# Kernel tuning notes

Measured on AMD Instinct MI355X. Metric: run time of the kernel, lower is better.

The kernel has to match this reference:

```python
import jax, jax.numpy as jnp
from jax import lax
import numpy as np

HEAD_SIZE = 64
D_MIX = 32
D_DECAY = 64
D_GATE = 64


def setup_inputs() -> dict:
    key = jax.random.key(0)
    B, T, C = 4, 2048, 1024
    H = C // HEAD_SIZE
    ks = jax.random.split(key, 24)
    n = lambda i, shape, s=1.0: (jax.random.normal(ks[i], shape, dtype=jnp.float32) * s)
    return {
        "x": n(0, (B, T, C)),
        "maa_x": n(1, (C,), 0.1), "maa_w": n(2, (C,), 0.1), "maa_k": n(3, (C,), 0.1),
        "maa_v": n(4, (C,), 0.1), "maa_r": n(5, (C,), 0.1), "maa_g": n(6, (C,), 0.1),
        "maa_w1": n(7, (C, 5 * D_MIX), 0.01), "maa_w2": n(8, (5, D_MIX, C), 0.01),
        "Wr": n(9, (C, C), C ** -0.5), "Wk": n(10, (C, C), C ** -0.5),
        "Wv": n(11, (C, C), C ** -0.5), "Wo": n(12, (C, C), C ** -0.5),
        "gate_w1": n(13, (C, D_GATE), 0.01), "gate_w2": n(14, (D_GATE, C), 0.01),
        "time_decay": n(15, (C,), 1.0) - 4.0,
        "decay_w1": n(16, (C, D_DECAY), 0.01), "decay_w2": n(17, (D_DECAY, C), 0.01),
        "u": n(18, (H, HEAD_SIZE), 0.1),
        "ln_g": jnp.ones((C,), jnp.float32), "ln_b": jnp.zeros((C,), jnp.float32),
    }


def _wkv6(r, k, v, w, u):
    # r,k,v: [B,T,C]; w: decay (already exp(-exp(.))) [B,T,C]; u: [H,N]
    B, T, C = r.shape
    N = HEAD_SIZE
    H = C // N
    to_h = lambda a: a.reshape(B, T, H, N).transpose(1, 0, 2, 3)  # [T,B,H,N]
    rT, kT, vT, wT = map(to_h, (r, k, v, w))

    def step(S, inp):  # S: [B,H,N,N] (key_dim i x value_dim j)
        rt, kt, vt, wt = inp
        kv = kt[..., :, None] * vt[..., None, :]            # [B,H,N,N]
        y = jnp.einsum('bhi,bhij->bhj', rt, S + u[None, :, :, None] * kv)
        S = wt[..., None] * S + kv
        return S, y

    S0 = jnp.zeros((B, H, N, N), r.dtype)
    _, y = lax.scan(step, S0, (rT, kT, vT, wT))
    return y.transpose(1, 0, 2, 3).reshape(B, T, C)


def reference(x, maa_x, maa_w, maa_k, maa_v, maa_r, maa_g, maa_w1, maa_w2,
              Wr, Wk, Wv, Wo, gate_w1, gate_w2, time_decay, decay_w1, decay_w2,
              u, ln_g, ln_b):
    B, T, C = x.shape
    H, N = C // HEAD_SIZE, HEAD_SIZE
    # time shift: prepend zero row, drop last (ZeroPad2d((0,0,1,-1)))
    xx = jnp.concatenate([jnp.zeros_like(x[:, :1]), x[:, :-1]], axis=1) - x
    xxx = x + xx * maa_x
    lora = jnp.tanh(xxx @ maa_w1).reshape(B, T, 5, D_MIX)
    m = jnp.einsum('btfd,fdc->fbtc', lora, maa_w2)  # [5,B,T,C]
    mw, mk, mv, mr, mg = m[0], m[1], m[2], m[3], m[4]
    xw = x + xx * (maa_w + mw)
    xk = x + xx * (maa_k + mk)
    xv = x + xx * (maa_v + mv)
    xr = x + xx * (maa_r + mr)
    xg = x + xx * (maa_g + mg)
    r = xr @ Wr
    k = xk @ Wk
    v = xv @ Wv
    g = jnp.tanh(xg @ gate_w1) @ gate_w2
    w = time_decay + jnp.tanh(xw @ decay_w1) @ decay_w2
    wdec = jnp.exp(-jnp.exp(w))  # decay applied inside the CUDA kernel
    y = _wkv6(r, k, v, wdec, u)
    # GroupNorm over heads, eps = 1e-5 * HEAD_SIZE_DIVISOR**2 = 6.4e-4
    yh = y.reshape(B, T, H, N)
    mu = yh.mean(-1, keepdims=True)
    var = yh.var(-1, keepdims=True)
    yn = ((yh - mu) / jnp.sqrt(var + 6.4e-4)).reshape(B, T, C) * ln_g + ln_b
    return (yn * g) @ Wo
```

## Files before the change

### kernel.cpp

```cpp
#include <hip/hip_runtime.h>
#include <hip/hip_bf16.h>
#include <stdint.h>

typedef __hip_bfloat16 bf16;
typedef __attribute__((ext_vector_type(8))) short bf16x8;
typedef __attribute__((ext_vector_type(4))) float f32x4;

#define CC 1024
#define TT 2048
#define BB 4
#define BT 8192
#define HH 16
#define NN 64

#define MFMA(a, b, c) __builtin_amdgcn_mfma_f32_16x16x32_bf16(a, b, c, 0, 0, 0)

#define GLD(g, l) __builtin_amdgcn_global_load_lds( \
    (const __attribute__((address_space(1))) void*)(g), \
    (__attribute__((address_space(3))) void*)(l), 16, 0, 0)

__device__ __forceinline__ short f2bs(float f) {
    bf16 h = __float2bfloat16(f);
    return *reinterpret_cast<short*>(&h);
}
__device__ __forceinline__ float bs2f(short s) {
    bf16 h = *reinterpret_cast<bf16*>(&s);
    return __bfloat162float(h);
}

__device__ __forceinline__ size_t blk_idx(int m, int k, int ktiles) {
    return ((size_t)(m >> 8) * ktiles + (k >> 6)) * 16384
         + ((k >> 3) & 7) * 2048 + (m & 255) * 8 + (k & 7);
}

__device__ __forceinline__ size_t blk128_idx(int m, int k, int ktiles) {
    return ((size_t)(m >> 7) * ktiles + (k >> 6)) * 8192
         + ((k >> 3) & 7) * 1024 + (m & 127) * 8 + (k & 7);
}

__device__ __forceinline__ size_t hb_idx(int m, int n) {
    return ((((size_t)(m >> 11) << 4) + (n >> 6)) * 2048 + (m & 2047)) * 64
         + (n & 63);
}

template <typename EPI>
__device__ __forceinline__ void gemm128(short* As, short* Bs,
                                        const bf16* __restrict__ A, int lda,
                                        const bf16* __restrict__ Bt, int ldb,
                                        int kiters, int m0, int n0, EPI epi)
{
    const int tid = threadIdx.x;
    const int l   = tid & 63, wv = tid >> 6;
    const int wm  = wv >> 1, wn = wv & 1;
    const int q   = l >> 4, lr = l & 15;
    const int row = tid & 127, kg1 = tid >> 7;

    f32x4 acc[4][4] = {};

    const bf16* ga = A  + (size_t)(m0 + row) * lda + kg1 * 8;
    const bf16* gb = Bt + (size_t)(n0 + row) * ldb + kg1 * 8;
    short* la1 = As + tid * 8;
    short* la2 = As + (tid + 256) * 8;
    short* lb1 = Bs + tid * 8;
    short* lb2 = Bs + (tid + 256) * 8;

    for (int kb = 0; kb < kiters; ++kb) {
        __syncthreads();
        const bf16* gak = ga + kb * 32;
        const bf16* gbk = gb + kb * 32;
        GLD(gak,      la1);
        GLD(gak + 16, la2);
        GLD(gbk,      lb1);
        GLD(gbk + 16, lb2);
        __syncthreads();
        bf16x8 af[4], bfb[4];
#pragma unroll
        for (int mt = 0; mt < 4; ++mt)
            af[mt] = *(const bf16x8*)(As + (q * 128 + wm * 64 + mt * 16 + lr) * 8);
#pragma unroll
        for (int nt = 0; nt < 4; ++nt)
            bfb[nt] = *(const bf16x8*)(Bs + (q * 128 + wn * 64 + nt * 16 + lr) * 8);
#pragma unroll
        for (int mt = 0; mt < 4; ++mt)
#pragma unroll
            for (int nt = 0; nt < 4; ++nt)
                acc[mt][nt] = MFMA(af[mt], bfb[nt], acc[mt][nt]);
    }
#pragma unroll
    for (int mt = 0; mt < 4; ++mt)
#pragma unroll
        for (int nt = 0; nt < 4; ++nt)
#pragma unroll
            for (int rr = 0; rr < 4; ++rr)
                epi(m0 + wm * 64 + mt * 16 + q * 4 + rr,
                    n0 + wn * 64 + nt * 16 + lr, acc[mt][nt][rr]);
}

template <typename EPI>
__device__ __forceinline__ void gemm128b(short* As, short* Bs,
                                         const bf16* __restrict__ A,
                                         const bf16* __restrict__ Bt,
                                         int kiters, int m0, int n0, EPI epi)
{
    const int tid = threadIdx.x;
    const int l   = tid & 63, wv = tid >> 6;
    const int wm  = wv >> 1, wn = wv & 1;
    const int q   = l >> 4, lr = l & 15;

    f32x4 acc[4][4] = {};

    const bf16* ga = A  + (size_t)(m0 >> 7) * 16 * 8192 + tid * 8;
    const bf16* gb = Bt + (size_t)(n0 >> 7) * 16 * 8192 + tid * 8;

    auto stage = [&](int kb, int u) {
        const bf16* gak = ga + (size_t)kb * 8192;
        const bf16* gbk = gb + (size_t)kb * 8192;
        short* la = As + u * 8192 + tid * 8;
        short* lb = Bs + u * 8192 + tid * 8;
        GLD(gak,        la);
        GLD(gak + 2048, la + 2048);
        GLD(gak + 4096, la + 4096);
        GLD(gak + 6144, la + 6144);
        GLD(gbk,        lb);
        GLD(gbk + 2048, lb + 2048);
        GLD(gbk + 4096, lb + 4096);
        GLD(gbk + 6144, lb + 6144);
    };

    __syncthreads();
    stage(0, 0);
    __syncthreads();
    for (int kb = 0; kb < kiters; ++kb) {
        const int cur = kb & 1;
        if (kb + 1 < kiters) stage(kb + 1, cur ^ 1);
        const short* Ac = As + cur * 8192;
        const short* Bc = Bs + cur * 8192;
        bf16x8 af[2][4], bfb[2][4];
#pragma unroll
        for (int hh = 0; hh < 2; ++hh) {
#pragma unroll
            for (int mt = 0; mt < 4; ++mt)
                af[hh][mt] = *(const bf16x8*)(Ac +
                    ((q + hh * 4) * 128 + wm * 64 + mt * 16 + lr) * 8);
#pragma unroll
            for (int nt = 0; nt < 4; ++nt)
                bfb[hh][nt] = *(const bf16x8*)(Bc +
                    ((q + hh * 4) * 128 + wn * 64 + nt * 16 + lr) * 8);
        }
        __builtin_amdgcn_s_setprio(1);
#pragma unroll
        for (int mt = 0; mt < 4; ++mt)
#pragma unroll
            for (int nt = 0; nt < 4; ++nt) {
                acc[mt][nt] = MFMA(af[0][mt], bfb[0][nt], acc[mt][nt]);
                acc[mt][nt] = MFMA(af[1][mt], bfb[1][nt], acc[mt][nt]);
            }
        __builtin_amdgcn_s_setprio(0);
        __syncthreads();
    }
#pragma unroll
    for (int mt = 0; mt < 4; ++mt)
#pragma unroll
        for (int nt = 0; nt < 4; ++nt)
#pragma unroll
            for (int rr = 0; rr < 4; ++rr)
                epi(m0 + wm * 64 + mt * 16 + q * 4 + rr,
                    n0 + wn * 64 + nt * 16 + lr, acc[mt][nt][rr]);
}

template <typename EPI>
__device__ __forceinline__ void gemm256(short* As, short* Bs,
                                        const bf16* __restrict__ A,
                                        const bf16* __restrict__ Bt,
                                        int kiters, int m0, int n0, EPI epi)
{
    const int tid = threadIdx.x;
    const int l   = tid & 63, wv = tid >> 6;
    const int wm  = wv >> 2, wn = wv & 3;
    const int q   = l >> 4, lr = l & 15;

    f32x4 acc[8][4] = {};

    const bf16* ga = A  + (size_t)(m0 >> 8) * 16 * 16384 + tid * 8;
    const bf16* gb = Bt + (size_t)(n0 >> 8) * 16 * 16384 + tid * 8;

    auto stage = [&](int kb, int u) {
        const bf16* gak = ga + (size_t)kb * 16384;
        const bf16* gbk = gb + (size_t)kb * 16384;
        short* la = As + u * 16384 + tid * 8;
        short* lb = Bs + u * 16384 + tid * 8;
        GLD(gak,         la);
        GLD(gak + 4096,  la + 4096);
        GLD(gak + 8192,  la + 8192);
        GLD(gak + 12288, la + 12288);
        GLD(gbk,         lb);
        GLD(gbk + 4096,  lb + 4096);
        GLD(gbk + 8192,  lb + 8192);
        GLD(gbk + 12288, lb + 12288);
    };

    __syncthreads();
    stage(0, 0);
    __syncthreads();
    for (int kb = 0; kb < kiters; ++kb) {
        const int cur = kb & 1;
        if (kb + 1 < kiters) stage(kb + 1, cur ^ 1);
        const short* Ac = As + cur * 16384;
        const short* Bc = Bs + cur * 16384;
#pragma unroll
        for (int hh = 0; hh < 2; ++hh) {
            bf16x8 af[8], bfb[4];
#pragma unroll
            for (int mt = 0; mt < 8; ++mt)
                af[mt] = *(const bf16x8*)(Ac +
                    ((q + hh * 4) * 256 + wm * 128 + mt * 16 + lr) * 8);
#pragma unroll
            for (int nt = 0; nt < 4; ++nt)
                bfb[nt] = *(const bf16x8*)(Bc +
                    ((q + hh * 4) * 256 + wn * 64 + nt * 16 + lr) * 8);
            __builtin_amdgcn_s_setprio(1);
#pragma unroll
            for (int mt = 0; mt < 8; ++mt)
#pragma unroll
                for (int nt = 0; nt < 4; ++nt)
                    acc[mt][nt] = MFMA(af[mt], bfb[nt], acc[mt][nt]);
            __builtin_amdgcn_s_setprio(0);
        }
        __syncthreads();
    }
#pragma unroll
    for (int mt = 0; mt < 8; ++mt)
#pragma unroll
        for (int nt = 0; nt < 4; ++nt)
#pragma unroll
            for (int rr = 0; rr < 4; ++rr)
                epi(m0 + wm * 128 + mt * 16 + q * 4 + rr,
                    n0 + wn * 64 + nt * 16 + lr, acc[mt][nt][rr]);
}

template <typename EPI>
__device__ __forceinline__ void gemmHid(short* As, short* Bs,
                                        const bf16* __restrict__ A,
                                        const bf16* __restrict__ Bt, int ldb,
                                        int kiters, int m0, EPI epi)
{
    const int tid = threadIdx.x;
    const int l   = tid & 63, wv = tid >> 6;
    const int q   = l >> 4, lr = l & 15;
    const int row64 = tid & 63, kg8 = tid >> 6;

    f32x4 acc[2][4] = {};

    const bf16* ga = A + (size_t)(m0 >> 8) * 16 * 16384 + tid * 8;
    const bf16* gb = Bt + (size_t)row64 * ldb + kg8 * 8;

    auto stage = [&](int kb, int u) {
        const bf16* gak = ga + (size_t)kb * 16384;
        short* la = As + u * 16384 + tid * 8;
        GLD(gak,         la);
        GLD(gak + 4096,  la + 4096);
        GLD(gak + 8192,  la + 8192);
        GLD(gak + 12288, la + 12288);
        GLD(gb + kb * 64, Bs + u * 4096 + tid * 8);
    };

    __syncthreads();
    stage(0, 0);
    __syncthreads();
    for (int kb = 0; kb < kiters; ++kb) {
        const int cur = kb & 1;
        if (kb + 1 < kiters) stage(kb + 1, cur ^ 1);
        const short* Ac = As + cur * 16384;
        const short* Bc = Bs + cur * 4096;
        bf16x8 af[2][2], bfb[2][4];
#pragma unroll
        for (int hh = 0; hh < 2; ++hh) {
#pragma unroll
            for (int mt = 0; mt < 2; ++mt)
                af[hh][mt] = *(const bf16x8*)(Ac +
                    ((q + hh * 4) * 256 + wv * 32 + mt * 16 + lr) * 8);
#pragma unroll
            for (int nt = 0; nt < 4; ++nt)
                bfb[hh][nt] = *(const bf16x8*)(Bc +
                    ((q + hh * 4) * 64 + nt * 16 + lr) * 8);
        }
#pragma unroll
        for (int mt = 0; mt < 2; ++mt)
#pragma unroll
            for (int nt = 0; nt < 4; ++nt) {
                acc[mt][nt] = MFMA(af[0][mt], bfb[0][nt], acc[mt][nt]);
                acc[mt][nt] = MFMA(af[1][mt], bfb[1][nt], acc[mt][nt]);
            }
        __syncthreads();
    }
#pragma unroll
    for (int mt = 0; mt < 2; ++mt)
#pragma unroll
        for (int nt = 0; nt < 4; ++nt)
#pragma unroll
            for (int rr = 0; rr < 4; ++rr)
                epi(m0 + wv * 32 + mt * 16 + q * 4 + rr,
                    nt * 16 + lr, acc[mt][nt][rr]);
}

__global__ __launch_bounds__(256) void k_prep_all(
    const float* __restrict__ Wr, const float* __restrict__ Wk,
    const float* __restrict__ Wv, const float* __restrict__ Wo,
    const float* __restrict__ maa_w1, const float* __restrict__ gate_w1,
    const float* __restrict__ decay_w1, const float* __restrict__ gate_w2,
    const float* __restrict__ decay_w2, const float* __restrict__ maa_w2,
    const float* __restrict__ mw, const float* __restrict__ mk,
    const float* __restrict__ mv, const float* __restrict__ mr,
    const float* __restrict__ mg, const float* __restrict__ x,
    const float* __restrict__ maa_x,
    bf16* __restrict__ WT3, bf16* __restrict__ WoT, bf16* __restrict__ w1T,
    bf16* __restrict__ w1T2, bf16* __restrict__ w2T2, bf16* __restrict__ w2T5,
    float* __restrict__ maas, bf16* __restrict__ xxx,
    bf16* __restrict__ xb, bf16* __restrict__ xxb)
{
    __shared__ float tile[32][33];
    int idx = blockIdx.x;
    if (idx >= 4900) {
        size_t i = ((size_t)(idx - 4900) * 256 + threadIdx.x) * 4;
        int cc = i & (CC - 1);
        int t  = (i >> 10) & (TT - 1);
        float4 xm = *(const float4*)(x + i);
        float4 xp = t ? *(const float4*)(x + i - CC)
                      : make_float4(0.f, 0.f, 0.f, 0.f);
        float4 ax = *(const float4*)(maa_x + cc);
        float xxv[4] = {xp.x - xm.x, xp.y - xm.y, xp.z - xm.z, xp.w - xm.w};
        float xmv[4] = {xm.x, xm.y, xm.z, xm.w};
        float axv[4] = {ax.x, ax.y, ax.z, ax.w};
#pragma unroll
        for (int e = 0; e < 4; ++e) {
            xb[i + e]  = __float2bfloat16(xmv[e]);
            xxb[i + e] = __float2bfloat16(xxv[e]);
            xxx[i + e] = __float2bfloat16(xmv[e] + xxv[e] * axv[e]);
        }
        return;
    }
    const float* src; bf16* dst; int rows, cols_in, tx_;
    int blkmode = 0;
    if (idx < 4096) {
        int s = idx >> 10; idx &= 1023;
        src = (s == 0) ? Wr : (s == 1) ? Wk : (s == 2) ? Wv : Wo;
        dst = (s == 3) ? WoT : WT3 + (size_t)s * CC * CC;
        blkmode = (s == 3) ? 2 : 1;
        rows = CC; cols_in = CC; tx_ = 32;
    } else if (idx < 4352) { idx -= 4096; src = maa_w1;  dst = w1T;  rows = CC; cols_in = 160; tx_ = 8; }
    else if (idx < 4480)   { idx -= 4352; src = gate_w1; dst = w1T2; rows = CC; cols_in = 64;  tx_ = 4; }
    else if (idx < 4608)   { idx -= 4480; src = decay_w1; dst = w1T2 + 128 * CC; rows = CC; cols_in = 64; tx_ = 4; }
    else if (idx < 4672)   { idx -= 4608; src = gate_w2;  dst = w2T2;           rows = 64; cols_in = CC; tx_ = 32; }
    else if (idx < 4736)   { idx -= 4672; src = decay_w2; dst = w2T2 + CC * 64; rows = 64; cols_in = CC; tx_ = 32; }
    else if (idx < 4896)   { idx -= 4736; int f = idx >> 5; idx &= 31;
                             src = maa_w2 + (size_t)f * 32 * CC;
                             dst = w2T5 + (size_t)f * CC * 32; rows = 32; cols_in = CC; tx_ = 32; }
    else {
        int i = (idx - 4896) * 256 + threadIdx.x;
        if (i < CC) {
            maas[i]          = mw[i];
            maas[CC + i]     = mk[i];
            maas[2 * CC + i] = mv[i];
            maas[3 * CC + i] = mr[i];
            maas[4 * CC + i] = mg[i];
        }
        return;
    }
    int bx = idx % tx_, by = idx / tx_;
    int c0 = bx * 32, r0 = by * 32;
    int tx = threadIdx.x & 31, ty = threadIdx.x >> 5;
    for (int i = ty; i < 32; i += 8) {
        int cc2 = c0 + tx;
        tile[i][tx] = (cc2 < cols_in) ? src[(size_t)(r0 + i) * cols_in + cc2] : 0.f;
    }
    __syncthreads();
    if (blkmode == 1) {
        for (int i = ty; i < 32; i += 8) {
            int R = c0 + i, C = r0 + tx;
            dst[blk_idx(R, C, 16)] = __float2bfloat16(tile[tx][i]);
        }
    } else if (blkmode == 2) {
        for (int i = ty; i < 32; i += 8) {
            int R = c0 + i, C = r0 + tx;
            dst[blk128_idx(R, C, 16)] = __float2bfloat16(tile[tx][i]);
        }
    } else {
        for (int i = ty; i < 32; i += 8)
            dst[(size_t)(c0 + i) * rows + r0 + tx] = __float2bfloat16(tile[tx][i]);
    }
}

__global__ __launch_bounds__(256) void g_lora(const bf16* __restrict__ xxx,
                                              const bf16* __restrict__ w1T,
                                              bf16* __restrict__ L)
{
    __shared__ __align__(16) short lds[8192];
    int m0 = blockIdx.x * 128, n0 = blockIdx.y * 128;
    gemm128(lds, lds + 4096, xxx, CC, w1T, CC, CC / 32, m0, n0,
            [&](int m, int n, float v) {
                if (n < 160) L[(size_t)m * 160 + n] = __float2bfloat16(tanhf(v));
            });
}

__global__ __launch_bounds__(256) void g_xvar(const bf16* __restrict__ L,
                                              const bf16* __restrict__ w2T,
                                              const float* __restrict__ maas,
                                              const bf16* __restrict__ xb,
                                              const bf16* __restrict__ xxb,
                                              bf16* __restrict__ xvars)
{
    __shared__ __align__(16) short lds[8192];
    int m0 = blockIdx.x * 128, n0 = blockIdx.y * 128;
    for (int f = 0; f < 5; ++f) {
        const bf16* A  = L + f * 32;
        const bf16* Bt = w2T + (size_t)f * CC * 32;
        const float* maa = maas + f * CC;
        bf16* out = xvars + (size_t)f * BT * CC;
        gemm128(lds, lds + 4096, A, 160, Bt, 32, 1, m0, n0,
                [&](int m, int n, float v) {
                    float xm = __bfloat162float(xb[(size_t)m * CC + n]);
                    float xx = __bfloat162float(xxb[(size_t)m * CC + n]);
                    out[blk_idx(m, n, 16)] =
                        __float2bfloat16(xm + xx * (maa[n] + v));
                });
    }
}

__global__ __launch_bounds__(512) void g_rkv5(const bf16* __restrict__ xvars,
                                              const bf16* __restrict__ WT,
                                              const bf16* __restrict__ w1T2,
                                              bf16* __restrict__ rkv,
                                              bf16* __restrict__ hid)
{
    __shared__ __align__(16) short lds[65536];
    int bid = blockIdx.x;
    if (bid < 384) {
        int swz = (bid & 7) * 48 + (bid >> 3);
        int z  = swz >> 7;
        int r2 = swz & 127;
        int n0 = (r2 >> 5) * 256;
        int m0 = (r2 & 31) * 256;
        int f = (z == 0) ? 3 : z;
        const bf16* A  = xvars + (size_t)f * BT * CC;
        const bf16* Bt = WT + (size_t)z * CC * CC;
        bf16* out = rkv + (size_t)z * BT * CC;
        gemm256(lds, lds + 32768, A, Bt, CC / 64, m0, n0,
                [&](int m, int n, float v) {
                    out[hb_idx(m, n)] = __float2bfloat16(v);
                });
    } else {
        int hb = bid - 384;
        int zz = hb >> 5, mi = hb & 31;
        const bf16* A  = xvars + (size_t)(zz == 0 ? 4 : 0) * BT * CC;
        const bf16* Bt = w1T2 + (size_t)zz * 128 * CC;
        bf16* out = hid + (size_t)zz * BT * 64;
        gemmHid(lds, lds + 32768, A, Bt, CC, CC / 64, mi * 256,
                [&](int m, int n, float v) {
                    out[(size_t)m * 64 + n] = __float2bfloat16(tanhf(v));
                });
    }
}

__global__ __launch_bounds__(256) void k_wkv_p1(const bf16* __restrict__ r,
                                                const bf16* __restrict__ kk,
                                                const bf16* __restrict__ vv,
                                                const bf16* __restrict__ hidW,
                                                const bf16* __restrict__ w2d,
                                                const float* __restrict__ td,
                                                const float* __restrict__ u,
                                                bf16* __restrict__ y,
                                                bf16* __restrict__ RTg,
                                                short* __restrict__ Mg,
                                                float* __restrict__ plg)
{
    constexpr int PW = 65, PB = 72;
    __shared__ __align__(16) char smem[16640 + 3 * 9216 + 768];
    float* LW = (float*)smem;
    short* VT = (short*)smem;
    short* RT = (short*)(smem + 16640);
    short* KT = (short*)(smem + 16640 + 9216);
    short* AT = KT;
    short* KH = (short*)(smem + 16640 + 2 * 9216);
    short* HT = KT;
    short* WD = KH;
    float* SU = (float*)(smem + 16640 + 3 * 9216);
    float* SD = SU + 64;

    const int tid = threadIdx.x;
    const int lane = tid & 63, wq = tid >> 6;
    const int row = tid >> 2, g = tid & 3, j0 = g * 16;
    const int l15 = lane & 15, q = lane >> 4;
    const int bh = blockIdx.x >> 5, c = blockIdx.x & 31;
    const int b = bh >> 4, h = bh & 15;
    const int t0 = c * 64;
    const int bt0 = b * TT + t0;
    const size_t hbb = (size_t)bh * TT * NN;
    const size_t cb = (size_t)blockIdx.x * 4096;

    if (tid < 64) SU[tid] = u[h * NN + tid];

#pragma unroll
    for (int rnd = 0; rnd < 2; ++rnd) {
        int ee = rnd * 256 + tid;
        int rw = ee >> 3, c8 = (ee & 7) * 8;
        *(bf16x8*)(HT + rw * PB + c8) =
            *(const bf16x8*)(hidW + (size_t)(bt0 + rw) * 64 + c8);
        *(bf16x8*)(WD + rw * PB + c8) =
            *(const bf16x8*)(w2d + (size_t)(h * 64 + rw) * 64 + c8);
    }
    const size_t gb = hbb + (size_t)(t0 + row) * 64 + j0;
    bf16x8 r0 = *(const bf16x8*)(r + gb),  r1 = *(const bf16x8*)(r + gb + 8);
    bf16x8 k0 = *(const bf16x8*)(kk + gb), k1 = *(const bf16x8*)(kk + gb + 8);
    bf16x8 v0 = *(const bf16x8*)(vv + gb), v1 = *(const bf16x8*)(vv + gb + 8);
    float tdv[4];
#pragma unroll
    for (int ct = 0; ct < 4; ++ct) tdv[ct] = td[h * 64 + ct * 16 + l15];
    __syncthreads();
    {
        bf16x8 aH0 = *(const bf16x8*)(HT + (wq * 16 + l15) * PB + q * 8);
        bf16x8 aH1 = *(const bf16x8*)(HT + (wq * 16 + l15) * PB + q * 8 + 32);
        f32x4 lwa[4] = {};
#pragma unroll
        for (int ct = 0; ct < 4; ++ct) {
            bf16x8 bW0 = *(const bf16x8*)(WD + (ct * 16 + l15) * PB + q * 8);
            bf16x8 bW1 = *(const bf16x8*)(WD + (ct * 16 + l15) * PB + q * 8 + 32);
            lwa[ct] = MFMA(aH0, bW0, lwa[ct]);
            lwa[ct] = MFMA(aH1, bW1, lwa[ct]);
        }
#pragma unroll
        for (int ct = 0; ct < 4; ++ct)
#pragma unroll
            for (int rr = 0; rr < 4; ++rr) {
                int t = wq * 16 + q * 4 + rr, j = ct * 16 + l15;
                LW[t * PW + j] = -expf(tdv[ct] + lwa[ct][rr]);
            }
    }
    __syncthreads();
    for (int jj = 0; jj < 16; ++jj) {
        int j = wq * 16 + jj;
        float xv = LW[lane * PW + j];
#pragma unroll
        for (int d = 1; d < 64; d <<= 1) {
            float t2 = __shfl_up(xv, d);
            if (lane >= d) xv += t2;
        }
        LW[lane * PW + j] = xv;
    }
    __syncthreads();
    float rF[16], kF[16];
#pragma unroll
    for (int c2 = 0; c2 < 8; ++c2) {
        rF[c2] = bs2f(r0[c2]); rF[8 + c2] = bs2f(r1[c2]);
        kF[c2] = bs2f(k0[c2]); kF[8 + c2] = bs2f(k1[c2]);
    }
    float cwp[16], cwm[16], cwL[16];
#pragma unroll
    for (int c2 = 0; c2 < 16; ++c2) {
        cwp[c2] = LW[row * PW + j0 + c2];
        cwm[c2] = row ? LW[(row - 1) * PW + j0 + c2] : 0.f;
        cwL[c2] = LW[63 * PW + j0 + c2];
    }
    bf16x8 w0, w1;
#pragma unroll
    for (int c2 = 0; c2 < 8; ++c2) {
        w0[c2] = f2bs(rF[c2] * expf(cwm[c2]));
        w1[c2] = f2bs(rF[8 + c2] * expf(cwm[8 + c2]));
    }
    *(bf16x8*)(RT + row * PB + j0)     = w0;
    *(bf16x8*)(RT + row * PB + j0 + 8) = w1;
    *(bf16x8*)((short*)RTg + cb + row * 64 + j0)     = w0;
    *(bf16x8*)((short*)RTg + cb + row * 64 + j0 + 8) = w1;
#pragma unroll
    for (int c2 = 0; c2 < 8; ++c2) {
        w0[c2] = f2bs(kF[c2] * expf(-cwp[c2]));
        w1[c2] = f2bs(kF[8 + c2] * expf(-cwp[8 + c2]));
    }
    *(bf16x8*)(KT + row * PB + j0)     = w0;
    *(bf16x8*)(KT + row * PB + j0 + 8) = w1;
#pragma unroll
    for (int c2 = 0; c2 < 16; ++c2)
        KH[(j0 + c2) * PB + row] = f2bs(kF[c2] * expf(cwL[c2] - cwp[c2]));
    if (tid < 64) plg[(size_t)blockIdx.x * 64 + tid] = expf(LW[63 * PW + tid]);
    float dpart = 0.f;
#pragma unroll
    for (int c2 = 0; c2 < 16; ++c2)
        dpart = fmaf(rF[c2] * kF[c2], SU[j0 + c2], dpart);
    dpart += __shfl_xor(dpart, 1);
    dpart += __shfl_xor(dpart, 2);
    if (g == 0) SD[row] = dpart;
    __syncthreads();
#pragma unroll
    for (int c2 = 0; c2 < 8; ++c2) {
        VT[(j0 + c2) * PB + row]     = v0[c2];
        VT[(j0 + 8 + c2) * PB + row] = v1[c2];
    }
    bf16x8 aF0 = *(const bf16x8*)(RT + (wq * 16 + l15) * PB + q * 8);
    bf16x8 aF1 = *(const bf16x8*)(RT + (wq * 16 + l15) * PB + q * 8 + 32);
    f32x4 Am[4] = {};
#pragma unroll
    for (int ct = 0; ct < 4; ++ct) {
        bf16x8 bF0 = *(const bf16x8*)(KT + (ct * 16 + l15) * PB + q * 8);
        bf16x8 bF1 = *(const bf16x8*)(KT + (ct * 16 + l15) * PB + q * 8 + 32);
        Am[ct] = MFMA(aF0, bF0, Am[ct]);
        Am[ct] = MFMA(aF1, bF1, Am[ct]);
    }
    __syncthreads();
#pragma unroll
    for (int ct = 0; ct < 4; ++ct)
#pragma unroll
        for (int rr = 0; rr < 4; ++rr) {
            int s = wq * 16 + q * 4 + rr, p = ct * 16 + l15;
            float vA = Am[ct][rr];
            vA = (p > s) ? 0.f : (p == s ? SD[s] : vA);
            AT[s * PB + p] = f2bs(vA);
        }
    __syncthreads();
    f32x4 Y[4] = {}, M[4] = {};
    bf16x8 aA0 = *(const bf16x8*)(AT + (wq * 16 + l15) * PB + q * 8);
    bf16x8 aA1 = *(const bf16x8*)(AT + (wq * 16 + l15) * PB + q * 8 + 32);
    bf16x8 aV0 = *(const bf16x8*)(VT + (wq * 16 + l15) * PB + q * 8);
    bf16x8 aV1 = *(const bf16x8*)(VT + (wq * 16 + l15) * PB + q * 8 + 32);
#pragma unroll
    for (int ct = 0; ct < 4; ++ct) {
        bf16x8 bV0 = *(const bf16x8*)(VT + (ct * 16 + l15) * PB + q * 8);
        bf16x8 bV1 = *(const bf16x8*)(VT + (ct * 16 + l15) * PB + q * 8 + 32);
        Y[ct] = MFMA(aA0, bV0, Y[ct]);
        Y[ct] = MFMA(aA1, bV1, Y[ct]);
        bf16x8 bK0 = *(const bf16x8*)(KH + (ct * 16 + l15) * PB + q * 8);
        bf16x8 bK1 = *(const bf16x8*)(KH + (ct * 16 + l15) * PB + q * 8 + 32);
        M[ct] = MFMA(aV0, bK0, M[ct]);
        M[ct] = MFMA(aV1, bK1, M[ct]);
    }
#pragma unroll
    for (int ct = 0; ct < 4; ++ct)
#pragma unroll
        for (int rr = 0; rr < 4; ++rr) {
            int s = wq * 16 + q * 4 + rr;
            y[hbb + (size_t)(t0 + s) * 64 + ct * 16 + l15] =
                __float2bfloat16(Y[ct][rr]);
            Mg[cb + (size_t)s * 64 + ct * 16 + l15] = f2bs(M[ct][rr]);
        }
}

__global__ __launch_bounds__(256) void k_wkv_p2(const short* __restrict__ Mg,
                                                const float* __restrict__ plg,
                                                bf16* __restrict__ Sg)
{
    int bh = blockIdx.x >> 4, part = blockIdx.x & 15;
    int i = part * 4 + (threadIdx.x >> 6), j = threadIdx.x & 63;
    float S = 0.f;
    size_t eb = (size_t)bh * 32 * 4096 + (size_t)i * 64 + j;
    size_t pb = (size_t)bh * 32 * 64 + j;
    for (int c = 0; c < 32; ++c) {
        Sg[eb + (size_t)c * 4096] = __float2bfloat16(S);
        S = plg[pb + (size_t)c * 64] * S + bs2f(Mg[eb + (size_t)c * 4096]);
    }
}

__global__ __launch_bounds__(256) void k_wkv_p3(const bf16* __restrict__ RTg,
                                                const bf16* __restrict__ Sg,
                                                const bf16* __restrict__ y,
                                                const bf16* __restrict__ hidG,
                                                const bf16* __restrict__ w2g,
                                                const float* __restrict__ ln_g,
                                                const float* __restrict__ ln_b,
                                                bf16* __restrict__ A2)
{
    constexpr int PB = 72;
    __shared__ __align__(16) short BufA[64 * PB], BufB[64 * PB];
    const int tid = threadIdx.x;
    const int lane = tid & 63, wq = tid >> 6;
    const int l15 = lane & 15, q = lane >> 4;
    const int bh = blockIdx.x >> 5, c = blockIdx.x & 31;
    const int b = bh >> 4, h = bh & 15;
    const int t0 = c * 64;
    const int bt0 = b * TT + t0;
    const size_t hbb = (size_t)bh * TT * NN;
    const size_t cb = (size_t)blockIdx.x * 4096;

#pragma unroll
    for (int rnd = 0; rnd < 2; ++rnd) {
        int ee = rnd * 256 + tid;
        int rw = ee >> 3, c8 = (ee & 7) * 8;
        *(bf16x8*)(BufA + rw * PB + c8) =
            *(const bf16x8*)(hidG + (size_t)(bt0 + rw) * 64 + c8);
        *(bf16x8*)(BufB + rw * PB + c8) =
            *(const bf16x8*)(w2g + (size_t)(h * 64 + rw) * 64 + c8);
    }
    __syncthreads();
    f32x4 G[4] = {};
    {
        bf16x8 aH0 = *(const bf16x8*)(BufA + (wq * 16 + l15) * PB + q * 8);
        bf16x8 aH1 = *(const bf16x8*)(BufA + (wq * 16 + l15) * PB + q * 8 + 32);
#pragma unroll
        for (int ct = 0; ct < 4; ++ct) {
            bf16x8 bW0 = *(const bf16x8*)(BufB + (ct * 16 + l15) * PB + q * 8);
            bf16x8 bW1 = *(const bf16x8*)(BufB + (ct * 16 + l15) * PB + q * 8 + 32);
            G[ct] = MFMA(aH0, bW0, G[ct]);
            G[ct] = MFMA(aH1, bW1, G[ct]);
        }
    }
    __syncthreads();
#pragma unroll
    for (int rnd = 0; rnd < 2; ++rnd) {
        int ee = rnd * 256 + tid;
        int rw = ee >> 3, c8 = (ee & 7) * 8;
        *(bf16x8*)(BufA + rw * PB + c8) =
            *(const bf16x8*)((const short*)RTg + cb + rw * 64 + c8);
        *(bf16x8*)(BufB + rw * PB + c8) =
            *(const bf16x8*)((const short*)Sg + cb + rw * 64 + c8);
    }
    __syncthreads();

    f32x4 Yc[4];
#pragma unroll
    for (int ct = 0; ct < 4; ++ct)
#pragma unroll
        for (int rr = 0; rr < 4; ++rr) {
            int s = wq * 16 + q * 4 + rr;
            Yc[ct][rr] = __bfloat162float(
                y[hbb + (size_t)(t0 + s) * 64 + ct * 16 + l15]);
        }
    bf16x8 aF0 = *(const bf16x8*)(BufA + (wq * 16 + l15) * PB + q * 8);
    bf16x8 aF1 = *(const bf16x8*)(BufA + (wq * 16 + l15) * PB + q * 8 + 32);
#pragma unroll
    for (int ct = 0; ct < 4; ++ct) {
        bf16x8 bS0 = *(const bf16x8*)(BufB + (ct * 16 + l15) * PB + q * 8);
        bf16x8 bS1 = *(const bf16x8*)(BufB + (ct * 16 + l15) * PB + q * 8 + 32);
        Yc[ct] = MFMA(aF0, bS0, Yc[ct]);
        Yc[ct] = MFMA(aF1, bS1, Yc[ct]);
    }
#pragma unroll
    for (int rr = 0; rr < 4; ++rr) {
        float s1 = 0.f, s2 = 0.f;
#pragma unroll
        for (int ct = 0; ct < 4; ++ct) {
            float vA = Yc[ct][rr];
            s1 += vA; s2 += vA * vA;
        }
#pragma unroll
        for (int o = 1; o < 16; o <<= 1) {
            s1 += __shfl_xor(s1, o);
            s2 += __shfl_xor(s2, o);
        }
        float mu  = s1 * (1.f / 64.f);
        float var = s2 * (1.f / 64.f) - mu * mu;
        float rstd = rsqrtf(var + 6.4e-4f);
        int s = wq * 16 + q * 4 + rr;
#pragma unroll
        for (int ct = 0; ct < 4; ++ct) {
            int ch = h * NN + ct * 16 + l15;
            float yn = (Yc[ct][rr] - mu) * rstd;
            float out = (yn * ln_g[ch] + ln_b[ch]) * G[ct][rr];
            A2[blk128_idx(bt0 + s, ch, 16)] = __float2bfloat16(out);
        }
    }
}

__global__ __launch_bounds__(256) void g_out(const bf16* __restrict__ A2,
                                             const bf16* __restrict__ WoT,
                                             float* __restrict__ out)
{
    __shared__ __align__(16) short lds[32768];
    int m0 = blockIdx.x * 128, n0 = blockIdx.y * 128;
    gemm128b(lds, lds + 16384, A2, WoT, CC / 64, m0, n0,
             [&](int m, int n, float v) { out[(size_t)m * CC + n] = v; });
}

extern "C" void kernel_launch(void* const* d_in, const int* in_sizes, int n_in,
                              void* d_out, int out_size, void* d_ws, size_t ws_size,
                              hipStream_t stream)
{
    const float* x        = (const float*)d_in[0];
    const float* maa_x    = (const float*)d_in[1];
    const float* maa_w    = (const float*)d_in[2];
    const float* maa_k    = (const float*)d_in[3];
    const float* maa_v    = (const float*)d_in[4];
    const float* maa_r    = (const float*)d_in[5];
    const float* maa_g    = (const float*)d_in[6];
    const float* maa_w1   = (const float*)d_in[7];
    const float* maa_w2   = (const float*)d_in[8];
    const float* Wr       = (const float*)d_in[9];
    const float* Wk       = (const float*)d_in[10];
    const float* Wv       = (const float*)d_in[11];
    const float* Wo       = (const float*)d_in[12];
    const float* gate_w1  = (const float*)d_in[13];
    const float* gate_w2  = (const float*)d_in[14];
    const float* time_dec = (const float*)d_in[15];
    const float* decay_w1 = (const float*)d_in[16];
    const float* decay_w2 = (const float*)d_in[17];
    const float* u        = (const float*)d_in[18];
    const float* ln_g     = (const float*)d_in[19];
    const float* ln_b     = (const float*)d_in[20];

    size_t off = 0;
    auto alloc = [&](size_t bytes) {
        off = (off + 255) & ~(size_t)255;
        void* p = (char*)d_ws + off;
        off += bytes;
        return p;
    };
    bf16*  WT3   = (bf16*) alloc(3ull * CC * CC * 2);
    bf16*  WoT   = (bf16*) alloc((size_t)CC * CC * 2);
    bf16*  w1T   = (bf16*) alloc(256ull * CC * 2);
    bf16*  w1T2  = (bf16*) alloc(2ull * 128 * CC * 2);
    bf16*  w2T2  = (bf16*) alloc(2ull * CC * 64 * 2);
    bf16*  w2T5  = (bf16*) alloc(5ull * CC * 32 * 2);
    float* maas  = (float*)alloc(5ull * CC * 4);
    char* bufA = (char*)alloc((size_t)BT * CC * 2);
    bf16* xxxbf = (bf16*)bufA;
    bf16* A2    = (bf16*)bufA;
    char* bufB = (char*)alloc((size_t)BT * 160 * 2);
    bf16* Lbf  = (bf16*)bufB;
    bf16* hid  = (bf16*)bufB;
    char* bufC = (char*)alloc(5ull * BT * CC * 2);
    bf16*  xvars = (bf16*)bufC;
    bf16*  ybuf  = (bf16*)bufC;
    bf16*  RTg   = (bf16*)(bufC + (size_t)BT * CC * 2);
    bf16*  rkv  = (bf16*)alloc(3ull * BT * CC * 2);
    bf16*  Sg   = rkv;
    bf16*  xb   = (bf16*) alloc((size_t)BT * CC * 2);
    bf16*  xxb  = (bf16*) alloc((size_t)BT * CC * 2);
    short* Mg   = (short*)alloc(64ull * 32 * 4096 * 2);
    float* plg  = (float*)alloc(64ull * 32 * 64 * 4);

    k_prep_all<<<dim3(13092), 256, 0, stream>>>(
        Wr, Wk, Wv, Wo, maa_w1, gate_w1, decay_w1, gate_w2, decay_w2, maa_w2,
        maa_w, maa_k, maa_v, maa_r, maa_g, x, maa_x,
        WT3, WoT, w1T, w1T2, w2T2, w2T5, maas, xxxbf, xb, xxb);

    g_lora<<<dim3(64, 2), 256, 0, stream>>>(xxxbf, w1T, Lbf);
    g_xvar<<<dim3(64, 8), 256, 0, stream>>>(Lbf, w2T5, maas, xb, xxb, xvars);
    g_rkv5<<<dim3(448), 512, 0, stream>>>(xvars, WT3, w1T2, rkv, hid);
    k_wkv_p1<<<dim3(2048), 256, 0, stream>>>(rkv, rkv + (size_t)BT * CC,
                                             rkv + 2ull * BT * CC,
                                             hid + (size_t)BT * 64,
                                             w2T2 + CC * 64,
                                             time_dec, u, ybuf, RTg, Mg, plg);
    k_wkv_p2<<<dim3(1024), 256, 0, stream>>>(Mg, plg, Sg);
    k_wkv_p3<<<dim3(2048), 256, 0, stream>>>(RTg, Sg, ybuf,
                                             hid,
                                             w2T2,
                                             ln_g, ln_b, A2);
    g_out<<<dim3(64, 8), 256, 0, stream>>>(A2, WoT, (float*)d_out);
}
```

Measured before the change: 394.2 us.

## Stage GEMM and WKV epilogue outputs through LDS for vectorized global stores

The epilogues of the r/k/v GEMM, the WKV chunk kernel and the GroupNorm/gate kernel previously wrote scattered 2-byte bf16 values straight to global memory. They now write accumulator values into padded LDS tiles, synchronize, and then emit coalesced 16-byte vector stores in the head-blocked or blk128 layouts. The aim is to reduce the number and scatter of global store transactions. In exchange the kernels use extra LDS, which enlarges the g_rkv5 shared allocation and may lower occupancy, and they add block-wide barriers.

Result: faster. 364.5 us (-7.5%).

```diff
diff --git a/kernel.cpp b/kernel.cpp
--- a/kernel.cpp
+++ b/kernel.cpp
@@ -36,11 +36,6 @@
 __device__ __forceinline__ size_t blk128_idx(int m, int k, int ktiles) {
     return ((size_t)(m >> 7) * ktiles + (k >> 6)) * 8192
          + ((k >> 3) & 7) * 1024 + (m & 127) * 8 + (k & 7);
-}
-
-__device__ __forceinline__ size_t hb_idx(int m, int n) {
-    return ((((size_t)(m >> 11) << 4) + (n >> 6)) * 2048 + (m & 2047)) * 64
-         + (n & 63);
 }
 
 template <typename EPI>
@@ -168,12 +163,14 @@
                     n0 + wn * 64 + nt * 16 + lr, acc[mt][nt][rr]);
 }
 
-template <typename EPI>
-__device__ __forceinline__ void gemm256(short* As, short* Bs,
+__device__ __forceinline__ void gemm256(short* lds,
                                         const bf16* __restrict__ A,
                                         const bf16* __restrict__ Bt,
-                                        int kiters, int m0, int n0, EPI epi)
-{
+                                        int kiters, int m0, int n0,
+                                        bf16* __restrict__ out)
+{
+    short* As = lds;
+    short* Bs = lds + 32768;
     const int tid = threadIdx.x;
     const int l   = tid & 63, wv = tid >> 6;
     const int wm  = wv >> 2, wn = wv & 3;
@@ -228,14 +225,33 @@
         }
         __syncthreads();
     }
+    constexpr int EP = 268;
+    short* E = lds;
 #pragma unroll
     for (int mt = 0; mt < 8; ++mt)
 #pragma unroll
         for (int nt = 0; nt < 4; ++nt)
 #pragma unroll
-            for (int rr = 0; rr < 4; ++rr)
-                epi(m0 + wm * 128 + mt * 16 + q * 4 + rr,
-                    n0 + wn * 64 + nt * 16 + lr, acc[mt][nt][rr]);
+            for (int rr = 0; rr < 4; ++rr) {
+                int r    = wm * 128 + mt * 16 + q * 4 + rr;
+                int ccol = wn * 64 + nt * 16 + lr;
+                E[r * EP + ccol] = f2bs(acc[mt][nt][rr]);
+            }
+    __syncthreads();
+    const int b     = m0 >> 11;
+    const int hbase = n0 >> 6;
+#pragma unroll
+    for (int it = 0; it < 16; ++it) {
+        int gidx = it * 512 + tid;
+        int hh   = gidx >> 11;
+        int u    = gidx & 2047;
+        int r    = u >> 3;
+        int cB   = (u & 7) * 8;
+        bf16x8 vdat = *(const bf16x8*)(E + r * EP + hh * 64 + cB);
+        size_t o = (((size_t)(b * 16 + hbase + hh)) * 2048
+                    + (size_t)((m0 & 2047) + r)) * 64 + cB;
+        *(bf16x8*)((short*)out + o) = vdat;
+    }
 }
 
 template <typename EPI>
@@ -432,7 +448,7 @@
                                               bf16* __restrict__ rkv,
                                               bf16* __restrict__ hid)
 {
-    __shared__ __align__(16) short lds[65536];
+    __shared__ __align__(16) short lds[68608];
     int bid = blockIdx.x;
     if (bid < 384) {
         int swz = (bid & 7) * 48 + (bid >> 3);
@@ -444,10 +460,7 @@
         const bf16* A  = xvars + (size_t)f * BT * CC;
         const bf16* Bt = WT + (size_t)z * CC * CC;
         bf16* out = rkv + (size_t)z * BT * CC;
-        gemm256(lds, lds + 32768, A, Bt, CC / 64, m0, n0,
-                [&](int m, int n, float v) {
-                    out[hb_idx(m, n)] = __float2bfloat16(v);
-                });
+        gemm256(lds, A, Bt, CC / 64, m0, n0, out);
     } else {
         int hb = bid - 384;
         int zz = hb >> 5, mi = hb & 31;
@@ -631,15 +644,23 @@
         M[ct] = MFMA(aV0, bK0, M[ct]);
         M[ct] = MFMA(aV1, bK1, M[ct]);
     }
+    __syncthreads();
 #pragma unroll
     for (int ct = 0; ct < 4; ++ct)
 #pragma unroll
         for (int rr = 0; rr < 4; ++rr) {
             int s = wq * 16 + q * 4 + rr;
-            y[hbb + (size_t)(t0 + s) * 64 + ct * 16 + l15] =
-                __float2bfloat16(Y[ct][rr]);
+            VT[s * PB + ct * 16 + l15] = f2bs(Y[ct][rr]);
             Mg[cb + (size_t)s * 64 + ct * 16 + l15] = f2bs(M[ct][rr]);
         }
+    __syncthreads();
+#pragma unroll
+    for (int it = 0; it < 2; ++it) {
+        int gidx = it * 256 + tid;
+        int rY = gidx >> 3, cB = (gidx & 7) * 8;
+        *(bf16x8*)((short*)y + hbb + (size_t)(t0 + rY) * 64 + cB) =
+            *(const bf16x8*)(VT + rY * PB + cB);
+    }
 }
 
 __global__ __launch_bounds__(256) void k_wkv_p2(const short* __restrict__ Mg,
@@ -730,6 +751,7 @@
         Yc[ct] = MFMA(aF0, bS0, Yc[ct]);
         Yc[ct] = MFMA(aF1, bS1, Yc[ct]);
     }
+    __syncthreads();
 #pragma unroll
     for (int rr = 0; rr < 4; ++rr) {
         float s1 = 0.f, s2 = 0.f;
@@ -751,8 +773,20 @@
         for (int ct = 0; ct < 4; ++ct) {
             int ch = h * NN + ct * 16 + l15;
             float yn = (Yc[ct][rr] - mu) * rstd;
-            float out = (yn * ln_g[ch] + ln_b[ch]) * G[ct][rr];
-            A2[blk128_idx(bt0 + s, ch, 16)] = __float2bfloat16(out);
+            float outv = (yn * ln_g[ch] + ln_b[ch]) * G[ct][rr];
+            BufA[s * PB + ct * 16 + l15] = f2bs(outv);
+        }
+    }
+    __syncthreads();
+    {
+        const size_t tb = ((size_t)((bt0) >> 7) * 16 + h) * 8192;
+        const int rowbase = bt0 & 127;
+#pragma unroll
+        for (int it = 0; it < 2; ++it) {
+            int gidx = it * 256 + tid;
+            int kg = gidx >> 6, rA = gidx & 63;
+            *(bf16x8*)((short*)A2 + tb + kg * 1024 + (size_t)(rowbase + rA) * 8) =
+                *(const bf16x8*)(BufA + rA * PB + kg * 8);
         }
     }
 }
```
